# Optimization experiments

Measured on AMD Instinct MI355X. Metric: run time of the kernel, lower is better.

The kernel has to match this reference:

```python
import jax, jax.numpy as jnp
import numpy as np

B, S, D = 2, 2048, 1024
H, DH = 16, 64  # num_head, head_dim; H*DH == D


def setup_inputs() -> dict:
    key = jax.random.key(0)
    ks = jax.random.split(key, 10)
    stdv = 1.0 / np.sqrt(D)
    def lin(k):
        kw, kb = jax.random.split(k)
        W = jax.random.uniform(kw, (D, D), jnp.float32, -stdv, stdv)
        b = jax.random.uniform(kb, (D,), jnp.float32, -stdv, stdv)
        return W, b
    Wq, bq = lin(ks[0]); Wk, bk = lin(ks[1]); Wv, bv = lin(ks[2]); Wo, bo = lin(ks[3])
    x = jax.random.normal(ks[4], (B, S, D), jnp.float32)
    # causal mask: True = attend
    mask = jnp.tril(jnp.ones((S, S), jnp.bool_))
    mask = jnp.broadcast_to(mask, (B, S, S))
    return {"x": x, "mask": mask, "Wq": Wq, "bq": bq, "Wk": Wk, "bk": bk,
            "Wv": Wv, "bv": bv, "Wo": Wo, "bo": bo}


def _split_head(t):
    # [B,S,D] -> [B*H, S, DH]
    return t.reshape(B, S, H, DH).transpose(0, 2, 1, 3).reshape(B * H, S, DH)


def _concat_head(t):
    # [B*H, S, DH] -> [B, S, D]
    return t.reshape(B, H, S, DH).transpose(0, 2, 1, 3).reshape(B, S, D)


def reference(x, mask, Wq, bq, Wk, bk, Wv, bv, Wo, bo):
    q = _split_head(x @ Wq.T + bq)
    k = _split_head(x @ Wk.T + bk)
    v = _split_head(x @ Wv.T + bv)
    scale = 1.0 / jnp.sqrt(jnp.float32(DH))
    # scores: [B, H, S, S], masked softmax (flash-attention math, unfused ref)
    scores = jnp.einsum('nqd,nkd->nqk', q, k).reshape(B, H, S, S) * scale
    scores = jnp.where(mask[:, None, :, :], scores, jnp.finfo(scores.dtype).min)
    attn = jax.nn.softmax(scores, axis=-1)
    out = jnp.einsum('bhqk,nkd->bhqd', attn, v.reshape(B, H, S, DH).reshape(B * H, S, DH)).reshape(B * H, S, DH) if False else jnp.einsum('nqk,nkd->nqd', attn.reshape(B * H, S, S), v)
    return _concat_head(out) @ Wo.T + bo
```

## Files before the change

### kernel.cpp

```cpp
#include <hip/hip_runtime.h>
#include <cstdint>

#define S_LEN  2048
#define NH     16
#define DHEAD  64
#define DMODEL 1024

typedef __bf16 bf16x8 __attribute__((ext_vector_type(8)));
typedef __bf16 bf16x2 __attribute__((ext_vector_type(2)));
typedef float  f32x4  __attribute__((ext_vector_type(4)));

__device__ __forceinline__ unsigned short f2bf(float x) {
  union { float f; unsigned int u; } c; c.f = x;
  unsigned int u = c.u;
  return (unsigned short)((u + 0x7fffu + ((u >> 16) & 1u)) >> 16);
}

__device__ __forceinline__ unsigned int pkbf(float a, float b) {
#if __has_builtin(__builtin_amdgcn_cvt_pk_bf16_f32)
  bf16x2 r = __builtin_amdgcn_cvt_pk_bf16_f32(a, b);
  return *(unsigned int*)&r;
#else
  return (unsigned int)f2bf(a) | ((unsigned int)f2bf(b) << 16);
#endif
}

__device__ __forceinline__ unsigned short f2bf1(float x) {
#if __has_builtin(__builtin_amdgcn_cvt_pk_bf16_f32)
  bf16x2 r = __builtin_amdgcn_cvt_pk_bf16_f32(x, x);
  union { bf16x2 v; unsigned int u; } c; c.v = r;
  return (unsigned short)(c.u & 0xffffu);
#else
  return f2bf(x);
#endif
}

__device__ __forceinline__ __bf16 us2bf(unsigned short u) {
  union { unsigned short u; __bf16 b; } c; c.u = u; return c.b;
}

__device__ __forceinline__ void glds16(const void* g, void* l) {
  __builtin_amdgcn_global_load_lds(
      (const __attribute__((address_space(1))) void*)g,
      (__attribute__((address_space(3))) void*)l, 16, 0, 0);
}

__device__ __forceinline__ f32x4 mfma16(bf16x8 a, bf16x8 b, f32x4 c) {
  return __builtin_amdgcn_mfma_f32_16x16x32_bf16(a, b, c, 0, 0, 0);
}

__global__ void cvt_all(const float* __restrict__ x,
                        const float* __restrict__ Wq,
                        const float* __restrict__ Wk,
                        const float* __restrict__ Wv,
                        const float* __restrict__ Wo,
                        unsigned short* __restrict__ xb,
                        unsigned short* __restrict__ wqkv,
                        unsigned short* __restrict__ wo) {
  const int b = blockIdx.x;
  const float* src;
  unsigned short* dst;
  int off;
  if (b < 4096)      { src = x;  dst = xb;                off = b; }
  else if (b < 5120) { src = Wq; dst = wqkv;              off = b - 4096; }
  else if (b < 6144) { src = Wk; dst = wqkv + (1 << 20);  off = b - 5120; }
  else if (b < 7168) { src = Wv; dst = wqkv + (2 << 20);  off = b - 6144; }
  else               { src = Wo; dst = wo;                off = b - 7168; }
  const int i = (off * 256 + threadIdx.x) * 4;
  float4 v = *(const float4*)&src[i];
  uint2 r;
  r.x = pkbf(v.x, v.y);
  r.y = pkbf(v.z, v.w);
  *(uint2*)&dst[i] = r;
}

template<int MODE, int BN>
__global__ __launch_bounds__(256)
void gemm_bt(const unsigned short* __restrict__ A,
             const unsigned short* __restrict__ W,
             const float* __restrict__ bias0,
             const float* __restrict__ bias1,
             const float* __restrict__ bias2,
             unsigned short* __restrict__ Qt,
             unsigned short* __restrict__ Kb,
             unsigned short* __restrict__ Vt,
             float* __restrict__ Out,
             int K) {
  constexpr int JN = BN / 32;
  __shared__ __align__(16) unsigned short As[2][128 * 32];
  __shared__ __align__(16) unsigned short Bs[2][BN * 32];
  const int t    = threadIdx.x;
  const int lane = t & 63;
  const int w    = t >> 6;
  const int lr   = lane & 15, lq = lane >> 4;
  const int wm   = (w >> 1) * 64, wn = (w & 1) * (BN / 2);
  const int m0   = blockIdx.y * 128, n0 = blockIdx.x * BN;
  const int ra   = t >> 2, ca = (t & 3) * 8;

  f32x4 acc[4][JN] = {};

  const int niter = K >> 6;
  for (int kk = 0; kk < niter; ++kk) {
    const int k0 = kk << 6;
#pragma unroll
    for (int kh = 0; kh < 2; ++kh) {
      const int kc = k0 + kh * 32;
      glds16(A + (m0 + ra) * K + kc + ca,      &As[kh][ra * 32 + ca]);
      glds16(A + (m0 + 64 + ra) * K + kc + ca, &As[kh][(64 + ra) * 32 + ca]);
      glds16(W + (n0 + ra) * K + kc + ca,      &Bs[kh][ra * 32 + ca]);
      if (BN == 128)
        glds16(W + (n0 + 64 + ra) * K + kc + ca, &Bs[kh][(64 + ra) * 32 + ca]);
    }
    __syncthreads();
#pragma unroll
    for (int kh = 0; kh < 2; ++kh) {
      bf16x8 af[4], bg[JN];
#pragma unroll
      for (int i = 0; i < 4; ++i)
        af[i] = *(const bf16x8*)&As[kh][(wm + i * 16 + lr) * 32 + lq * 8];
#pragma unroll
      for (int j = 0; j < JN; ++j)
        bg[j] = *(const bf16x8*)&Bs[kh][(wn + j * 16 + lr) * 32 + lq * 8];
#pragma unroll
      for (int i = 0; i < 4; ++i)
#pragma unroll
        for (int j = 0; j < JN; ++j)
          acc[i][j] = mfma16(af[i], bg[j], acc[i][j]);
    }
    __syncthreads();
  }

  if (MODE == 0) {
    const int tsel = n0 >> 10;
#pragma unroll
    for (int i = 0; i < 4; ++i) {
#pragma unroll
      for (int j = 0; j < JN; ++j) {
        const int mb = m0 + wm + i * 16 + lq * 4;
        const int n  = n0 + wn + j * 16 + lr;
        const int d  = n & 1023;
        const int bidx = mb >> 11, s = mb & (S_LEN - 1);
        const int h = d >> 6, dh = d & 63;
        const int bh = bidx * NH + h;
        const float bv0 = (tsel == 0) ? bias0[d] : ((tsel == 1) ? bias1[d] : bias2[d]);
        if (tsel == 0) {
          const float sc = 0.125f * 1.44269504088896f;
          uint2 pv;
          pv.x = pkbf((acc[i][j][0] + bv0) * sc, (acc[i][j][1] + bv0) * sc);
          pv.y = pkbf((acc[i][j][2] + bv0) * sc, (acc[i][j][3] + bv0) * sc);
          *(uint2*)&Qt[(bh * DHEAD + dh) * S_LEN + s] = pv;
        } else if (tsel == 2) {
          uint2 pv;
          pv.x = pkbf(acc[i][j][0] + bv0, acc[i][j][1] + bv0);
          pv.y = pkbf(acc[i][j][2] + bv0, acc[i][j][3] + bv0);
          *(uint2*)&Vt[(bh * DHEAD + dh) * S_LEN + s] = pv;
        } else {
#pragma unroll
          for (int r = 0; r < 4; ++r)
            Kb[(bh * S_LEN + s + r) * DHEAD + dh] = f2bf1(acc[i][j][r] + bv0);
        }
      }
    }
  } else {
#pragma unroll
    for (int i = 0; i < 4; ++i)
#pragma unroll
      for (int j = 0; j < JN; ++j)
#pragma unroll
        for (int r = 0; r < 4; ++r) {
          const int m = m0 + wm + i * 16 + lq * 4 + r;
          const int n = n0 + wn + j * 16 + lr;
          Out[m * DMODEL + n] = acc[i][j][r] + bias0[n];
        }
  }
}

__global__ __launch_bounds__(256, 4)
void flash_kernel(const unsigned short* __restrict__ Qt,
                  const unsigned short* __restrict__ Kb,
                  const unsigned short* __restrict__ Vt,
                  unsigned short* __restrict__ Ocat) {
  __shared__ __align__(16) unsigned short Ks[2][2][64 * 32];
  __shared__ __align__(16) unsigned short Vs[2][2][64 * 32];
  __shared__ __align__(16) unsigned short pls[4][1024];
  const int w = threadIdx.x >> 6, lane = threadIdx.x & 63;
  const int lr = lane & 15, lq = lane >> 4;
  const int bh = blockIdx.x;
  const int sb = 31 - blockIdx.y;
  const char* Kc = (const char*)(Kb + bh * (S_LEN * DHEAD));
  const char* Vc = (const char*)(Vt + bh * (DHEAD * S_LEN));
  const unsigned short* Qp = Qt + bh * (DHEAD * S_LEN);
  const int bb = bh >> 4, h = bh & 15;
  unsigned short* pw = &pls[w][0];
  const int swz = lr & 7;

  const int hh  = w & 1;
  const int rbb = (w >> 1) * 2;
  const int rlane = lane >> 2;
  const int clane = (lane & 3) * 16;

  const int q0 = sb * 64 + w * 16;
  bf16x8 qlo, qhi;
#pragma unroll
  for (int j = 0; j < 8; ++j) {
    qlo[j] = us2bf(Qp[(lq * 8 + j) * S_LEN + q0 + lr]);
    qhi[j] = us2bf(Qp[(32 + lq * 8 + j) * S_LEN + q0 + lr]);
  }

  bf16x8 ones;
#pragma unroll
  for (int j = 0; j < 8; ++j) ones[j] = (__bf16)1.0f;

  f32x4 o[4] = {};
  f32x4 lacc = {};
  const int nfull = sb;

  auto stage = [&](int buf, int sk0) {
#pragma unroll
    for (int j = 0; j < 2; ++j) {
      const int rb = rbb + j;
      glds16(Kc + (sk0 + rb * 16 + rlane) * 128 + hh * 64 + clane,
             &Ks[buf][hh][rb * 16 * 32]);
      glds16(Vc + (rb * 16 + rlane) * 4096 + (sk0 + hh * 32) * 2 + clane,
             &Vs[buf][hh][rb * 16 * 32]);
    }
  };

  stage(0, 0);
  for (int kt = 0; kt <= nfull; ++kt) {
    const int buf = kt & 1;
    __syncthreads();
    if (kt < nfull) stage(1 - buf, (kt + 1) << 6);

    f32x4 st[4] = {};
    const unsigned short* Kl = Ks[buf][0];
    const unsigned short* Kh = Ks[buf][1];
#pragma unroll
    for (int t = 0; t < 4; ++t) {
      st[t] = mfma16(*(const bf16x8*)&Kl[(t * 16 + lr) * 32 + lq * 8], qlo, st[t]);
      st[t] = mfma16(*(const bf16x8*)&Kh[(t * 16 + lr) * 32 + lq * 8], qhi, st[t]);
    }
    float p[4][4];
#pragma unroll
    for (int t = 0; t < 4; ++t)
#pragma unroll
      for (int r = 0; r < 4; ++r)
        p[t][r] = __builtin_amdgcn_exp2f(st[t][r]);
    if (kt == nfull) {
      const int q = q0 + lr, sk0 = kt << 6;
#pragma unroll
      for (int t = 0; t < 4; ++t)
#pragma unroll
        for (int r = 0; r < 4; ++r) {
          const int k = sk0 + t * 16 + lq * 4 + r;
          if (k > q) p[t][r] = 0.f;
        }
    }

#pragma unroll
    for (int t = 0; t < 4; ++t) {
      uint2 pk;
      pk.x = pkbf(p[t][0], p[t][1]);
      pk.y = pkbf(p[t][2], p[t][3]);
      const int g = t * 2 + (lq >> 1);
      *(uint2*)&pw[lr * 64 + ((g ^ swz) << 3) + ((lq & 1) << 2)] = pk;
    }
    const bf16x8 pf0 = *(const bf16x8*)&pw[lr * 64 + ((lq ^ swz) << 3)];
    const bf16x8 pf1 = *(const bf16x8*)&pw[lr * 64 + (((4 + lq) ^ swz) << 3)];
    const unsigned short* Vl = Vs[buf][0];
    const unsigned short* Vh = Vs[buf][1];
#pragma unroll
    for (int tt = 0; tt < 4; ++tt) {
      o[tt] = mfma16(*(const bf16x8*)&Vl[(tt * 16 + lr) * 32 + lq * 8], pf0, o[tt]);
      o[tt] = mfma16(*(const bf16x8*)&Vh[(tt * 16 + lr) * 32 + lq * 8], pf1, o[tt]);
    }
    lacc = mfma16(ones, pf0, lacc);
    lacc = mfma16(ones, pf1, lacc);
  }

  const float inv = 1.f / lacc[0];
#pragma unroll
  for (int tt = 0; tt < 4; ++tt) {
    uint2 ov;
    ov.x = pkbf(o[tt][0] * inv, o[tt][1] * inv);
    ov.y = pkbf(o[tt][2] * inv, o[tt][3] * inv);
    *(uint2*)&Ocat[(bb * S_LEN + q0 + lr) * DMODEL + h * DHEAD + tt * 16 + lq * 4] = ov;
  }
}

extern "C" void kernel_launch(void* const* d_in, const int* in_sizes, int n_in,
                              void* d_out, int out_size, void* d_ws, size_t ws_size,
                              hipStream_t stream) {
  const float* x  = (const float*)d_in[0];
  const float* Wq = (const float*)d_in[2];
  const float* bq = (const float*)d_in[3];
  const float* Wk = (const float*)d_in[4];
  const float* bk = (const float*)d_in[5];
  const float* Wv = (const float*)d_in[6];
  const float* bv = (const float*)d_in[7];
  const float* Wo = (const float*)d_in[8];
  const float* bo = (const float*)d_in[9];
  float* out = (float*)d_out;

  char* ws = (char*)d_ws;
  unsigned short* xb   = (unsigned short*)(ws);
  unsigned short* wqkv = (unsigned short*)(ws + (8ull  << 20));
  unsigned short* wo   = (unsigned short*)(ws + (14ull << 20));
  unsigned short* Qt   = (unsigned short*)(ws + (16ull << 20));
  unsigned short* Kb   = (unsigned short*)(ws + (24ull << 20));
  unsigned short* Vt   = (unsigned short*)(ws + (32ull << 20));
  unsigned short* Ocat = (unsigned short*)(ws + (40ull << 20));

  cvt_all<<<8192, 256, 0, stream>>>(x, Wq, Wk, Wv, Wo, xb, wqkv, wo);

  gemm_bt<0, 128><<<dim3(24, 32), 256, 0, stream>>>(xb, wqkv, bq, bk, bv,
                                                    Qt, Kb, Vt, nullptr, 1024);
  flash_kernel<<<dim3(32, 32), 256, 0, stream>>>(Qt, Kb, Vt, Ocat);
  gemm_bt<1, 64><<<dim3(16, 32), 256, 0, stream>>>(Ocat, wo, bo, nullptr, nullptr,
                                                   nullptr, nullptr, nullptr, out, 1024);
}
```

Measured before the change: 203.7 us.

## Pair causal query blocks per workgroup and reuse K/V fragments across four query sets

The flash kernel now uses 2-wave workgroups, each handling two query blocks (sbA and 31-sbA), so every workgroup does the same total causal work. Each wave holds four 16-row query sets in registers and loads the K/V fragments from LDS once per tile, then reuses them across the sets. This cuts LDS traffic and K/V global staging per query row and evens out load across workgroups. In exchange, register pressure rises (16 output accumulators plus Q fragments), there are half as many workgroups with fewer waves each, and the inner set loop has a variable trip count.

Measured after the change: 742.4 us. 3.64x slower.

```diff
diff --git a/kernel.cpp b/kernel.cpp
--- a/kernel.cpp
+++ b/kernel.cpp
@@ -175,18 +175,19 @@
   }
 }
 
-__global__ __launch_bounds__(256, 4)
+__global__ __launch_bounds__(128, 2)
 void flash_kernel(const unsigned short* __restrict__ Qt,
                   const unsigned short* __restrict__ Kb,
                   const unsigned short* __restrict__ Vt,
                   unsigned short* __restrict__ Ocat) {
   __shared__ __align__(16) unsigned short Ks[2][2][64 * 32];
   __shared__ __align__(16) unsigned short Vs[2][2][64 * 32];
-  __shared__ __align__(16) unsigned short pls[4][1024];
+  __shared__ __align__(16) unsigned short pls[2][1024];
   const int w = threadIdx.x >> 6, lane = threadIdx.x & 63;
   const int lr = lane & 15, lq = lane >> 4;
   const int bh = blockIdx.x;
-  const int sb = 31 - blockIdx.y;
+  const int sbA = blockIdx.y;
+  const int sbB = 31 - sbA;
   const char* Kc = (const char*)(Kb + bh * (S_LEN * DHEAD));
   const char* Vc = (const char*)(Vt + bh * (DHEAD * S_LEN));
   const unsigned short* Qp = Qt + bh * (DHEAD * S_LEN);
@@ -194,97 +195,116 @@
   unsigned short* pw = &pls[w][0];
   const int swz = lr & 7;
 
-  const int hh  = w & 1;
-  const int rbb = (w >> 1) * 2;
   const int rlane = lane >> 2;
   const int clane = (lane & 3) * 16;
 
-  const int q0 = sb * 64 + w * 16;
-  bf16x8 qlo, qhi;
-#pragma unroll
-  for (int j = 0; j < 8; ++j) {
-    qlo[j] = us2bf(Qp[(lq * 8 + j) * S_LEN + q0 + lr]);
-    qhi[j] = us2bf(Qp[(32 + lq * 8 + j) * S_LEN + q0 + lr]);
-  }
+  int qbase[4], diag[4];
+  qbase[0] = sbB * 64 + w * 32;      diag[0] = sbB;
+  qbase[1] = qbase[0] + 16;          diag[1] = sbB;
+  qbase[2] = sbA * 64 + w * 32;      diag[2] = sbA;
+  qbase[3] = qbase[2] + 16;          diag[3] = sbA;
+
+  bf16x8 qf[4][2];
+#pragma unroll
+  for (int s = 0; s < 4; ++s)
+#pragma unroll
+    for (int j = 0; j < 8; ++j) {
+      qf[s][0][j] = us2bf(Qp[(lq * 8 + j) * S_LEN + qbase[s] + lr]);
+      qf[s][1][j] = us2bf(Qp[(32 + lq * 8 + j) * S_LEN + qbase[s] + lr]);
+    }
 
   bf16x8 ones;
 #pragma unroll
   for (int j = 0; j < 8; ++j) ones[j] = (__bf16)1.0f;
 
-  f32x4 o[4] = {};
-  f32x4 lacc = {};
-  const int nfull = sb;
+  f32x4 o[4][4] = {};
+  f32x4 lacc[4] = {};
 
   auto stage = [&](int buf, int sk0) {
 #pragma unroll
-    for (int j = 0; j < 2; ++j) {
-      const int rb = rbb + j;
-      glds16(Kc + (sk0 + rb * 16 + rlane) * 128 + hh * 64 + clane,
-             &Ks[buf][hh][rb * 16 * 32]);
-      glds16(Vc + (rb * 16 + rlane) * 4096 + (sk0 + hh * 32) * 2 + clane,
-             &Vs[buf][hh][rb * 16 * 32]);
+    for (int rb = 0; rb < 4; ++rb) {
+      glds16(Kc + (sk0 + rb * 16 + rlane) * 128 + w * 64 + clane,
+             &Ks[buf][w][rb * 512]);
+      glds16(Vc + (rb * 16 + rlane) * 4096 + (sk0 + w * 32) * 2 + clane,
+             &Vs[buf][w][rb * 512]);
     }
   };
 
   stage(0, 0);
-  for (int kt = 0; kt <= nfull; ++kt) {
+  for (int kt = 0; kt <= sbB; ++kt) {
     const int buf = kt & 1;
     __syncthreads();
-    if (kt < nfull) stage(1 - buf, (kt + 1) << 6);
-
-    f32x4 st[4] = {};
+    if (kt < sbB) stage(1 - buf, (kt + 1) << 6);
+
+    bf16x8 kfl[4], kfh[4], vfl[4], vfh[4];
     const unsigned short* Kl = Ks[buf][0];
     const unsigned short* Kh = Ks[buf][1];
-#pragma unroll
-    for (int t = 0; t < 4; ++t) {
-      st[t] = mfma16(*(const bf16x8*)&Kl[(t * 16 + lr) * 32 + lq * 8], qlo, st[t]);
-      st[t] = mfma16(*(const bf16x8*)&Kh[(t * 16 + lr) * 32 + lq * 8], qhi, st[t]);
-    }
-    float p[4][4];
-#pragma unroll
-    for (int t = 0; t < 4; ++t)
-#pragma unroll
-      for (int r = 0; r < 4; ++r)
-        p[t][r] = __builtin_amdgcn_exp2f(st[t][r]);
-    if (kt == nfull) {
-      const int q = q0 + lr, sk0 = kt << 6;
-#pragma unroll
-      for (int t = 0; t < 4; ++t)
-#pragma unroll
-        for (int r = 0; r < 4; ++r) {
-          const int k = sk0 + t * 16 + lq * 4 + r;
-          if (k > q) p[t][r] = 0.f;
-        }
-    }
-
-#pragma unroll
-    for (int t = 0; t < 4; ++t) {
-      uint2 pk;
-      pk.x = pkbf(p[t][0], p[t][1]);
-      pk.y = pkbf(p[t][2], p[t][3]);
-      const int g = t * 2 + (lq >> 1);
-      *(uint2*)&pw[lr * 64 + ((g ^ swz) << 3) + ((lq & 1) << 2)] = pk;
-    }
-    const bf16x8 pf0 = *(const bf16x8*)&pw[lr * 64 + ((lq ^ swz) << 3)];
-    const bf16x8 pf1 = *(const bf16x8*)&pw[lr * 64 + (((4 + lq) ^ swz) << 3)];
     const unsigned short* Vl = Vs[buf][0];
     const unsigned short* Vh = Vs[buf][1];
 #pragma unroll
+    for (int t = 0; t < 4; ++t) {
+      kfl[t] = *(const bf16x8*)&Kl[(t * 16 + lr) * 32 + lq * 8];
+      kfh[t] = *(const bf16x8*)&Kh[(t * 16 + lr) * 32 + lq * 8];
+      vfl[t] = *(const bf16x8*)&Vl[(t * 16 + lr) * 32 + lq * 8];
+      vfh[t] = *(const bf16x8*)&Vh[(t * 16 + lr) * 32 + lq * 8];
+    }
+
+    const int nsets = (kt <= sbA) ? 4 : 2;
+    const int sk0 = kt << 6;
+    for (int s = 0; s < nsets; ++s) {
+      f32x4 st[4] = {};
+#pragma unroll
+      for (int t = 0; t < 4; ++t) {
+        st[t] = mfma16(kfl[t], qf[s][0], st[t]);
+        st[t] = mfma16(kfh[t], qf[s][1], st[t]);
+      }
+      float p[4][4];
+#pragma unroll
+      for (int t = 0; t < 4; ++t)
+#pragma unroll
+        for (int r = 0; r < 4; ++r)
+          p[t][r] = __builtin_amdgcn_exp2f(st[t][r]);
+      if (kt == diag[s]) {
+        const int q = qbase[s] + lr;
+#pragma unroll
+        for (int t = 0; t < 4; ++t)
+#pragma unroll
+          for (int r = 0; r < 4; ++r) {
+            const int k = sk0 + t * 16 + lq * 4 + r;
+            if (k > q) p[t][r] = 0.f;
+          }
+      }
+
+#pragma unroll
+      for (int t = 0; t < 4; ++t) {
+        uint2 pk;
+        pk.x = pkbf(p[t][0], p[t][1]);
+        pk.y = pkbf(p[t][2], p[t][3]);
+        const int g = t * 2 + (lq >> 1);
+        *(uint2*)&pw[lr * 64 + ((g ^ swz) << 3) + ((lq & 1) << 2)] = pk;
+      }
+      const bf16x8 pf0 = *(const bf16x8*)&pw[lr * 64 + ((lq ^ swz) << 3)];
+      const bf16x8 pf1 = *(const bf16x8*)&pw[lr * 64 + (((4 + lq) ^ swz) << 3)];
+#pragma unroll
+      for (int tt = 0; tt < 4; ++tt) {
+        o[s][tt] = mfma16(vfl[tt], pf0, o[s][tt]);
+        o[s][tt] = mfma16(vfh[tt], pf1, o[s][tt]);
+      }
+      lacc[s] = mfma16(ones, pf0, lacc[s]);
+      lacc[s] = mfma16(ones, pf1, lacc[s]);
+    }
+  }
+
+#pragma unroll
+  for (int s = 0; s < 4; ++s) {
+    const float inv = 1.f / lacc[s][0];
+#pragma unroll
     for (int tt = 0; tt < 4; ++tt) {
-      o[tt] = mfma16(*(const bf16x8*)&Vl[(tt * 16 + lr) * 32 + lq * 8], pf0, o[tt]);
-      o[tt] = mfma16(*(const bf16x8*)&Vh[(tt * 16 + lr) * 32 + lq * 8], pf1, o[tt]);
-    }
-    lacc = mfma16(ones, pf0, lacc);
-    lacc = mfma16(ones, pf1, lacc);
-  }
-
-  const float inv = 1.f / lacc[0];
-#pragma unroll
-  for (int tt = 0; tt < 4; ++tt) {
-    uint2 ov;
-    ov.x = pkbf(o[tt][0] * inv, o[tt][1] * inv);
-    ov.y = pkbf(o[tt][2] * inv, o[tt][3] * inv);
-    *(uint2*)&Ocat[(bb * S_LEN + q0 + lr) * DMODEL + h * DHEAD + tt * 16 + lq * 4] = ov;
+      uint2 ov;
+      ov.x = pkbf(o[s][tt][0] * inv, o[s][tt][1] * inv);
+      ov.y = pkbf(o[s][tt][2] * inv, o[s][tt][3] * inv);
+      *(uint2*)&Ocat[(bb * S_LEN + qbase[s] + lr) * DMODEL + h * DHEAD + tt * 16 + lq * 4] = ov;
+    }
   }
 }
 
@@ -315,7 +335,7 @@
 
   gemm_bt<0, 128><<<dim3(24, 32), 256, 0, stream>>>(xb, wqkv, bq, bk, bv,
                                                     Qt, Kb, Vt, nullptr, 1024);
-  flash_kernel<<<dim3(32, 32), 256, 0, stream>>>(Qt, Kb, Vt, Ocat);
+  flash_kernel<<<dim3(32, 16), 128, 0, stream>>>(Qt, Kb, Vt, Ocat);
   gemm_bt<1, 64><<<dim3(16, 32), 256, 0, stream>>>(Ocat, wo, bo, nullptr, nullptr,
                                                    nullptr, nullptr, nullptr, out, 1024);
 }
```
